# Performance work log

Hardware: AMD Instinct MI355X
Metric: run time of the kernel (lower is better)

Reference implementation:

```python
import jax, jax.numpy as jnp
import numpy as np
from jax import lax

WIN = 9
PAD = WIN // 2


def _box_sum(x):
    # x: [B,1,H,W]; all-ones WINxWIN conv, stride 1, pad PAD -> same spatial size
    k = jnp.ones((1, 1, WIN, WIN), dtype=x.dtype)
    return lax.conv_general_dilated(
        x, k, window_strides=(1, 1), padding=[(PAD, PAD), (PAD, PAD)],
        dimension_numbers=("NCHW", "OIHW", "NCHW"))


def setup_inputs() -> dict:
    key = jax.random.key(0)
    k1, k2 = jax.random.split(key)
    B, C, H, W = 32, 1, 512, 512
    y_true = jax.random.uniform(k1, (B, C, H, W), dtype=jnp.float32)
    y_pred = jax.random.uniform(k2, (B, C, H, W), dtype=jnp.float32)
    return {"y_true": y_true, "y_pred": y_pred}


def reference(y_true, y_pred):
    Ii, Ji = y_true, y_pred
    win_size = float(WIN * WIN)
    I_sum = _box_sum(Ii)
    J_sum = _box_sum(Ji)
    I2_sum = _box_sum(Ii * Ii)
    J2_sum = _box_sum(Ji * Ji)
    IJ_sum = _box_sum(Ii * Ji)
    u_I = I_sum / win_size
    u_J = J_sum / win_size
    cross = IJ_sum - u_J * I_sum - u_I * J_sum + u_I * u_J * win_size
    I_var = I2_sum - 2.0 * u_I * I_sum + u_I * u_I * win_size
    J_var = J2_sum - 2.0 * u_J * J_sum + u_J * u_J * win_size
    cc = cross * cross / (I_var * J_var + 1e-05)
    return -jnp.mean(cc)
```

## Files before the change

kernel.cpp:

```cpp
#include <hip/hip_runtime.h>


#define BATCH     32
#define IMH       512
#define IMW       512
#define SH        16
#define NROWSTRIP 32
#define NCOLSTRIP 4
#define CBW       128
#define NPART     (BATCH * NROWSTRIP * NCOLSTRIP)
#define NK        (SH + 8)
#define VROW      136

#define LOADROW(RI, CI, CJ, HI, HJ) do {                                   \
    const int ri_ = (RI);                                                  \
    CI = make_float2(0.f, 0.f); CJ = make_float2(0.f, 0.f);                \
    HI = 0.f; HJ = 0.f;                                                    \
    if ((unsigned)ri_ < (unsigned)IMH) {                                   \
        const float* rI_ = Ib + (size_t)ri_ * IMW;                         \
        const float* rJ_ = Jb + (size_t)ri_ * IMW;                         \
        CI = *(const float2*)(rI_ + cc0);                                  \
        CJ = *(const float2*)(rJ_ + cc0);                                  \
        if (u < 8 && (unsigned)hc < (unsigned)IMW) {                       \
            HI = rI_[hc]; HJ = rJ_[hc];                                    \
        }                                                                  \
    }                                                                      \
} while (0)

#define HWIN(QI, HA, HB) do {                                              \
    const float2 w0_ = *(const float2*)&Vbuf[QI][l0];                      \
    const float2 w1_ = *(const float2*)&Vbuf[QI][l0 + 2];                  \
    const float2 w2_ = *(const float2*)&Vbuf[QI][l0 + 4];                  \
    const float2 w3_ = *(const float2*)&Vbuf[QI][l0 + 6];                  \
    const float2 w4_ = *(const float2*)&Vbuf[QI][l0 + 8];                  \
    HA = ((w0_.x + w0_.y) + (w1_.x + w1_.y))                               \
       + ((w2_.x + w2_.y) + (w3_.x + w3_.y)) + w4_.x;                      \
    HB = HA + w4_.y - w0_.x;                                               \
} while (0)

#define CC1(AI, AJ, S2, S3, S4) do {                                       \
    const float cross = (S4) - (AI)*(AJ)*inv81;                            \
    const float ivv   = (S2) - (AI)*(AI)*inv81;                            \
    const float jvv   = (S3) - (AJ)*(AJ)*inv81;                            \
    acc += cross * cross * __builtin_amdgcn_rcpf(ivv * jvv + 1e-5f);       \
} while (0)

__global__ __launch_bounds__(64) void ncc_main(const float* __restrict__ I,
                                               const float* __restrict__ J,
                                               float* __restrict__ partial) {
    const int u    = threadIdx.x;
    const int cs   = blockIdx.x;
    const int s    = blockIdx.y;
    const int b    = blockIdx.z;
    const int r0   = s * SH;
    const int cblk = cs * CBW;
    const int cc0  = cblk + 2 * u;
    const int hc   = cblk + (u < 4 ? u - 4 : 124 + u);
    const int hx   = (u < 4) ? u : 128 + u;
    const int l0   = 2 * u;
    const float inv81 = 1.0f / 81.0f;

    const float* Ib = I + (size_t)b * IMH * IMW;
    const float* Jb = J + (size_t)b * IMH * IMW;

    __shared__ float4 ring[9][64];
    __shared__ float2 ringH[9][8];
    __shared__ float  Vbuf[5][VROW];

    float VI0 = 0.f, VI1 = 0.f, VJ0 = 0.f, VJ1 = 0.f;
    float VII0 = 0.f, VII1 = 0.f, VJJ0 = 0.f, VJJ1 = 0.f;
    float VIJ0 = 0.f, VIJ1 = 0.f;
    float hVI = 0.f, hVJ = 0.f, hVII = 0.f, hVJJ = 0.f, hVIJ = 0.f;
    float acc = 0.f;
    int slot = 0;

    float2 ci, cj; float hi, hj;
    LOADROW(r0 - 4, ci, cj, hi, hj);

#pragma unroll 1
    for (int K = 0; K < NK; ++K) {
        float2 ni, nj; float nhi, nhj;
        LOADROW((K + 1 < NK) ? (r0 - 3 + K) : -1, ni, nj, nhi, nhj);

        float4 oldv = make_float4(0.f, 0.f, 0.f, 0.f);
        float2 oldh = make_float2(0.f, 0.f);
        if (K >= 9) {
            oldv = ring[slot][u];
            if (u < 8) oldh = ringH[slot][u];
        }
        ring[slot][u] = make_float4(ci.x, ci.y, cj.x, cj.y);
        if (u < 8) ringH[slot][u] = make_float2(hi, hj);
        slot = (slot == 8) ? 0 : slot + 1;

        VI0  += ci.x - oldv.x;             VI1  += ci.y - oldv.y;
        VJ0  += cj.x - oldv.z;             VJ1  += cj.y - oldv.w;
        VII0 += ci.x*ci.x - oldv.x*oldv.x; VII1 += ci.y*ci.y - oldv.y*oldv.y;
        VJJ0 += cj.x*cj.x - oldv.z*oldv.z; VJJ1 += cj.y*cj.y - oldv.w*oldv.w;
        VIJ0 += ci.x*cj.x - oldv.x*oldv.z; VIJ1 += ci.y*cj.y - oldv.y*oldv.w;
        hVI  += hi - oldh.x;               hVJ  += hj - oldh.y;
        hVII += hi*hi - oldh.x*oldh.x;
        hVJJ += hj*hj - oldh.y*oldh.y;
        hVIJ += hi*hj - oldh.x*oldh.y;

        if (K >= 8) {
            *(float2*)&Vbuf[0][4 + l0] = make_float2(VI0,  VI1);
            *(float2*)&Vbuf[1][4 + l0] = make_float2(VJ0,  VJ1);
            *(float2*)&Vbuf[2][4 + l0] = make_float2(VII0, VII1);
            *(float2*)&Vbuf[3][4 + l0] = make_float2(VJJ0, VJJ1);
            *(float2*)&Vbuf[4][4 + l0] = make_float2(VIJ0, VIJ1);
            if (u < 8) {
                Vbuf[0][hx] = hVI;  Vbuf[1][hx] = hVJ;  Vbuf[2][hx] = hVII;
                Vbuf[3][hx] = hVJJ; Vbuf[4][hx] = hVIJ;
            }
            __syncthreads();
            float HI0, HI1, HJ0, HJ1, HA0, HA1, HB0, HB1, HC0, HC1;
            HWIN(0, HI0, HI1);
            HWIN(1, HJ0, HJ1);
            HWIN(2, HA0, HA1);
            HWIN(3, HB0, HB1);
            HWIN(4, HC0, HC1);
            CC1(HI0, HJ0, HA0, HB0, HC0);
            CC1(HI1, HJ1, HA1, HB1, HC1);
            __syncthreads();
        }

        ci = ni; cj = nj; hi = nhi; hj = nhj;
    }

    float sum = acc;
#pragma unroll
    for (int off = 32; off > 0; off >>= 1) sum += __shfl_down(sum, off, 64);
    if (u == 0) {
        partial[((size_t)b * NROWSTRIP + s) * NCOLSTRIP + cs] = sum;
    }
}

__global__ __launch_bounds__(256) void ncc_reduce(const float* __restrict__ partial,
                                                  float* __restrict__ out) {
    const int t = threadIdx.x;
    double ssum = 0.0;
    for (int idx = t; idx < NPART; idx += 256) ssum += (double)partial[idx];
#pragma unroll
    for (int off = 32; off > 0; off >>= 1) ssum += __shfl_down(ssum, off, 64);

    __shared__ double wsum[4];
    if ((t & 63) == 0) wsum[t >> 6] = ssum;
    __syncthreads();
    if (t == 0) {
        const double total = wsum[0] + wsum[1] + wsum[2] + wsum[3];
        out[0] = (float)(-total / 8388608.0);
    }
}

extern "C" void kernel_launch(void* const* d_in, const int* in_sizes, int n_in,
                              void* d_out, int out_size, void* d_ws, size_t ws_size,
                              hipStream_t stream) {
    const float* I = (const float*)d_in[0];
    const float* J = (const float*)d_in[1];
    float* partial = (float*)d_ws;
    float* out     = (float*)d_out;

    dim3 grid(NCOLSTRIP, NROWSTRIP, BATCH);
    ncc_main<<<grid, 64, 0, stream>>>(I, J, partial);
    ncc_reduce<<<1, 256, 0, stream>>>(partial, out);
}
```

Baseline: 126.8 us.

## Stage full row tile in LDS once and do horizontal-then-vertical box sums

Replaces the streaming ring-buffer scheme, which had two barriers per output row, with a single bulk load of all 24 input rows (interleaved I/J as float2) into shared memory followed by one barrier. Each output row then computes horizontal window sums from LDS and keeps vertical sums as a sliding add/subtract in registers. Horizontal sums for each row are recomputed twice (once entering, once leaving the window), trading extra ALU and LDS reads for the removed syncs. It also sets launch_bounds min blocks to 1 and fully unrolls, which can raise register pressure.

```diff
diff --git a/kernel.cpp b/kernel.cpp
--- a/kernel.cpp
+++ b/kernel.cpp
@@ -8,34 +8,34 @@
 #define NROWSTRIP 32
 #define NCOLSTRIP 4
 #define CBW       128
+#define NK        (SH + 8)
+#define TW        136
 #define NPART     (BATCH * NROWSTRIP * NCOLSTRIP)
-#define NK        (SH + 8)
-#define VROW      136
 
-#define LOADROW(RI, CI, CJ, HI, HJ) do {                                   \
-    const int ri_ = (RI);                                                  \
-    CI = make_float2(0.f, 0.f); CJ = make_float2(0.f, 0.f);                \
-    HI = 0.f; HJ = 0.f;                                                    \
-    if ((unsigned)ri_ < (unsigned)IMH) {                                   \
-        const float* rI_ = Ib + (size_t)ri_ * IMW;                         \
-        const float* rJ_ = Jb + (size_t)ri_ * IMW;                         \
-        CI = *(const float2*)(rI_ + cc0);                                  \
-        CJ = *(const float2*)(rJ_ + cc0);                                  \
-        if (u < 8 && (unsigned)hc < (unsigned)IMW) {                       \
-            HI = rI_[hc]; HJ = rJ_[hc];                                    \
-        }                                                                  \
-    }                                                                      \
-} while (0)
-
-#define HWIN(QI, HA, HB) do {                                              \
-    const float2 w0_ = *(const float2*)&Vbuf[QI][l0];                      \
-    const float2 w1_ = *(const float2*)&Vbuf[QI][l0 + 2];                  \
-    const float2 w2_ = *(const float2*)&Vbuf[QI][l0 + 4];                  \
-    const float2 w3_ = *(const float2*)&Vbuf[QI][l0 + 6];                  \
-    const float2 w4_ = *(const float2*)&Vbuf[QI][l0 + 8];                  \
-    HA = ((w0_.x + w0_.y) + (w1_.x + w1_.y))                               \
-       + ((w2_.x + w2_.y) + (w3_.x + w3_.y)) + w4_.x;                      \
-    HB = HA + w4_.y - w0_.x;                                               \
+#define HCALC(K, HI0,HI1,HJ0,HJ1,HA0,HA1,HB0,HB1,HC0,HC1) do {             \
+    const float4 w0_ = *(const float4*)&tile[K][l0];                       \
+    const float4 w1_ = *(const float4*)&tile[K][l0 + 2];                   \
+    const float4 w2_ = *(const float4*)&tile[K][l0 + 4];                   \
+    const float4 w3_ = *(const float4*)&tile[K][l0 + 6];                   \
+    const float4 w4_ = *(const float4*)&tile[K][l0 + 8];                   \
+    HI0 = ((w0_.x + w0_.z) + (w1_.x + w1_.z))                              \
+        + ((w2_.x + w2_.z) + (w3_.x + w3_.z)) + w4_.x;                     \
+    HI1 = HI0 + w4_.z - w0_.x;                                             \
+    HJ0 = ((w0_.y + w0_.w) + (w1_.y + w1_.w))                              \
+        + ((w2_.y + w2_.w) + (w3_.y + w3_.w)) + w4_.y;                     \
+    HJ1 = HJ0 + w4_.w - w0_.y;                                             \
+    HA0 = ((w0_.x*w0_.x + w0_.z*w0_.z) + (w1_.x*w1_.x + w1_.z*w1_.z))      \
+        + ((w2_.x*w2_.x + w2_.z*w2_.z) + (w3_.x*w3_.x + w3_.z*w3_.z))      \
+        + w4_.x*w4_.x;                                                     \
+    HA1 = HA0 + w4_.z*w4_.z - w0_.x*w0_.x;                                 \
+    HB0 = ((w0_.y*w0_.y + w0_.w*w0_.w) + (w1_.y*w1_.y + w1_.w*w1_.w))      \
+        + ((w2_.y*w2_.y + w2_.w*w2_.w) + (w3_.y*w3_.y + w3_.w*w3_.w))      \
+        + w4_.y*w4_.y;                                                     \
+    HB1 = HB0 + w4_.w*w4_.w - w0_.y*w0_.y;                                 \
+    HC0 = ((w0_.x*w0_.y + w0_.z*w0_.w) + (w1_.x*w1_.y + w1_.z*w1_.w))      \
+        + ((w2_.x*w2_.y + w2_.z*w2_.w) + (w3_.x*w3_.y + w3_.z*w3_.w))      \
+        + w4_.x*w4_.y;                                                     \
+    HC1 = HC0 + w4_.z*w4_.w - w0_.x*w0_.y;                                 \
 } while (0)
 
 #define CC1(AI, AJ, S2, S3, S4) do {                                       \
@@ -45,86 +45,77 @@
     acc += cross * cross * __builtin_amdgcn_rcpf(ivv * jvv + 1e-5f);       \
 } while (0)
 
-__global__ __launch_bounds__(64) void ncc_main(const float* __restrict__ I,
-                                               const float* __restrict__ J,
-                                               float* __restrict__ partial) {
+__global__ __launch_bounds__(64, 1) void ncc_main(const float* __restrict__ I,
+                                                  const float* __restrict__ J,
+                                                  float* __restrict__ partial) {
     const int u    = threadIdx.x;
     const int cs   = blockIdx.x;
     const int s    = blockIdx.y;
     const int b    = blockIdx.z;
     const int r0   = s * SH;
     const int cblk = cs * CBW;
-    const int cc0  = cblk + 2 * u;
-    const int hc   = cblk + (u < 4 ? u - 4 : 124 + u);
-    const int hx   = (u < 4) ? u : 128 + u;
+    const int stc  = cblk - 4 + 2 * u;
+    const int hc   = cblk + 124 + u;
     const int l0   = 2 * u;
     const float inv81 = 1.0f / 81.0f;
 
     const float* Ib = I + (size_t)b * IMH * IMW;
     const float* Jb = J + (size_t)b * IMH * IMW;
 
-    __shared__ float4 ring[9][64];
-    __shared__ float2 ringH[9][8];
-    __shared__ float  Vbuf[5][VROW];
+    __shared__ float2 tile[NK][TW];
 
-    float VI0 = 0.f, VI1 = 0.f, VJ0 = 0.f, VJ1 = 0.f;
-    float VII0 = 0.f, VII1 = 0.f, VJJ0 = 0.f, VJJ1 = 0.f;
-    float VIJ0 = 0.f, VIJ1 = 0.f;
-    float hVI = 0.f, hVJ = 0.f, hVII = 0.f, hVJJ = 0.f, hVIJ = 0.f;
+#pragma unroll
+    for (int k = 0; k < NK; ++k) {
+        const int ri = r0 - 4 + k;
+        float2 iv = make_float2(0.f, 0.f), jv = make_float2(0.f, 0.f);
+        float hi = 0.f, hj = 0.f;
+        if ((unsigned)ri < (unsigned)IMH) {
+            const float* rI = Ib + (size_t)ri * IMW;
+            const float* rJ = Jb + (size_t)ri * IMW;
+            if ((unsigned)stc < (unsigned)IMW) {
+                iv = *(const float2*)(rI + stc);
+                jv = *(const float2*)(rJ + stc);
+            }
+            if (u < 8 && (unsigned)hc < (unsigned)IMW) {
+                hi = rI[hc]; hj = rJ[hc];
+            }
+        }
+        *(float4*)&tile[k][2 * u] = make_float4(iv.x, jv.x, iv.y, jv.y);
+        if (u < 8) tile[k][128 + u] = make_float2(hi, hj);
+    }
+    __syncthreads();
+
+    float vI0 = 0.f, vI1 = 0.f, vJ0 = 0.f, vJ1 = 0.f;
+    float vA0 = 0.f, vA1 = 0.f, vB0 = 0.f, vB1 = 0.f;
+    float vC0 = 0.f, vC1 = 0.f;
     float acc = 0.f;
-    int slot = 0;
 
-    float2 ci, cj; float hi, hj;
-    LOADROW(r0 - 4, ci, cj, hi, hj);
+    {
+        float hI0, hI1, hJ0, hJ1, hA0, hA1, hB0, hB1, hC0, hC1;
+#pragma unroll
+        for (int k = 0; k < 9; ++k) {
+            HCALC(k, hI0, hI1, hJ0, hJ1, hA0, hA1, hB0, hB1, hC0, hC1);
+            vI0 += hI0; vI1 += hI1; vJ0 += hJ0; vJ1 += hJ1;
+            vA0 += hA0; vA1 += hA1; vB0 += hB0; vB1 += hB1;
+            vC0 += hC0; vC1 += hC1;
+        }
+        CC1(vI0, vJ0, vA0, vB0, vC0);
+        CC1(vI1, vJ1, vA1, vB1, vC1);
+    }
 
-#pragma unroll 1
-    for (int K = 0; K < NK; ++K) {
-        float2 ni, nj; float nhi, nhj;
-        LOADROW((K + 1 < NK) ? (r0 - 3 + K) : -1, ni, nj, nhi, nhj);
-
-        float4 oldv = make_float4(0.f, 0.f, 0.f, 0.f);
-        float2 oldh = make_float2(0.f, 0.f);
-        if (K >= 9) {
-            oldv = ring[slot][u];
-            if (u < 8) oldh = ringH[slot][u];
-        }
-        ring[slot][u] = make_float4(ci.x, ci.y, cj.x, cj.y);
-        if (u < 8) ringH[slot][u] = make_float2(hi, hj);
-        slot = (slot == 8) ? 0 : slot + 1;
-
-        VI0  += ci.x - oldv.x;             VI1  += ci.y - oldv.y;
-        VJ0  += cj.x - oldv.z;             VJ1  += cj.y - oldv.w;
-        VII0 += ci.x*ci.x - oldv.x*oldv.x; VII1 += ci.y*ci.y - oldv.y*oldv.y;
-        VJJ0 += cj.x*cj.x - oldv.z*oldv.z; VJJ1 += cj.y*cj.y - oldv.w*oldv.w;
-        VIJ0 += ci.x*cj.x - oldv.x*oldv.z; VIJ1 += ci.y*cj.y - oldv.y*oldv.w;
-        hVI  += hi - oldh.x;               hVJ  += hj - oldh.y;
-        hVII += hi*hi - oldh.x*oldh.x;
-        hVJJ += hj*hj - oldh.y*oldh.y;
-        hVIJ += hi*hj - oldh.x*oldh.y;
-
-        if (K >= 8) {
-            *(float2*)&Vbuf[0][4 + l0] = make_float2(VI0,  VI1);
-            *(float2*)&Vbuf[1][4 + l0] = make_float2(VJ0,  VJ1);
-            *(float2*)&Vbuf[2][4 + l0] = make_float2(VII0, VII1);
-            *(float2*)&Vbuf[3][4 + l0] = make_float2(VJJ0, VJJ1);
-            *(float2*)&Vbuf[4][4 + l0] = make_float2(VIJ0, VIJ1);
-            if (u < 8) {
-                Vbuf[0][hx] = hVI;  Vbuf[1][hx] = hVJ;  Vbuf[2][hx] = hVII;
-                Vbuf[3][hx] = hVJJ; Vbuf[4][hx] = hVIJ;
-            }
-            __syncthreads();
-            float HI0, HI1, HJ0, HJ1, HA0, HA1, HB0, HB1, HC0, HC1;
-            HWIN(0, HI0, HI1);
-            HWIN(1, HJ0, HJ1);
-            HWIN(2, HA0, HA1);
-            HWIN(3, HB0, HB1);
-            HWIN(4, HC0, HC1);
-            CC1(HI0, HJ0, HA0, HB0, HC0);
-            CC1(HI1, HJ1, HA1, HB1, HC1);
-            __syncthreads();
-        }
-
-        ci = ni; cj = nj; hi = nhi; hj = nhj;
+#pragma unroll
+    for (int t = 1; t < SH; ++t) {
+        float nI0, nI1, nJ0, nJ1, nA0, nA1, nB0, nB1, nC0, nC1;
+        float oI0, oI1, oJ0, oJ1, oA0, oA1, oB0, oB1, oC0, oC1;
+        HCALC(t + 8, nI0, nI1, nJ0, nJ1, nA0, nA1, nB0, nB1, nC0, nC1);
+        HCALC(t - 1, oI0, oI1, oJ0, oJ1, oA0, oA1, oB0, oB1, oC0, oC1);
+        vI0 += nI0 - oI0; vI1 += nI1 - oI1;
+        vJ0 += nJ0 - oJ0; vJ1 += nJ1 - oJ1;
+        vA0 += nA0 - oA0; vA1 += nA1 - oA1;
+        vB0 += nB0 - oB0; vB1 += nB1 - oB1;
+        vC0 += nC0 - oC0; vC1 += nC1 - oC1;
+        CC1(vI0, vJ0, vA0, vB0, vC0);
+        CC1(vI1, vJ1, vA1, vB1, vC1);
     }
 
     float sum = acc;
```

New measurement: 150.6 us. 18.8% more time.

## Deepen row prefetch to four rows and double strip height

Applied to the files above, without the earlier changes.

Each block now processes 32 output rows instead of 16, which halves the grid and cuts the redundant 8-row halo recomputation per strip. The loop is unrolled by four, with four register-held row buffers so global loads for rows K+4..K+7 are in flight while rows K..K+3 are processed, hiding memory latency. This costs more registers and gives fewer blocks, which lowers parallelism across CUs.

```diff
diff --git a/kernel.cpp b/kernel.cpp
--- a/kernel.cpp
+++ b/kernel.cpp
@@ -4,19 +4,20 @@
 #define BATCH     32
 #define IMH       512
 #define IMW       512
-#define SH        16
-#define NROWSTRIP 32
+#define SH        32
+#define NROWSTRIP 16
 #define NCOLSTRIP 4
 #define CBW       128
-#define NPART     (BATCH * NROWSTRIP * NCOLSTRIP)
 #define NK        (SH + 8)
 #define VROW      136
+#define NPART     (BATCH * NROWSTRIP * NCOLSTRIP)
 
-#define LOADROW(RI, CI, CJ, HI, HJ) do {                                   \
-    const int ri_ = (RI);                                                  \
+#define PREFG(KK, CI, CJ, HI, HJ) do {                                     \
+    const int kk_ = (KK);                                                  \
+    const int ri_ = r0 - 4 + kk_;                                          \
     CI = make_float2(0.f, 0.f); CJ = make_float2(0.f, 0.f);                \
     HI = 0.f; HJ = 0.f;                                                    \
-    if ((unsigned)ri_ < (unsigned)IMH) {                                   \
+    if (kk_ < NK && (unsigned)ri_ < (unsigned)IMH) {                       \
         const float* rI_ = Ib + (size_t)ri_ * IMW;                         \
         const float* rJ_ = Jb + (size_t)ri_ * IMW;                         \
         CI = *(const float2*)(rI_ + cc0);                                  \
@@ -45,6 +46,50 @@
     acc += cross * cross * __builtin_amdgcn_rcpf(ivv * jvv + 1e-5f);       \
 } while (0)
 
+#define EMIT() do {                                                        \
+    *(float2*)&Vbuf[0][4 + l0] = make_float2(VI0, VI1);                    \
+    *(float2*)&Vbuf[1][4 + l0] = make_float2(VJ0, VJ1);                    \
+    *(float2*)&Vbuf[2][4 + l0] = make_float2(VA0, VA1);                    \
+    *(float2*)&Vbuf[3][4 + l0] = make_float2(VB0, VB1);                    \
+    *(float2*)&Vbuf[4][4 + l0] = make_float2(VC0, VC1);                    \
+    if (u < 8) {                                                           \
+        Vbuf[0][hx] = hVI; Vbuf[1][hx] = hVJ; Vbuf[2][hx] = hVA;           \
+        Vbuf[3][hx] = hVB; Vbuf[4][hx] = hVC;                              \
+    }                                                                      \
+    __syncthreads();                \
+    float HI0, HI1, HJ0, HJ1, HA0, HA1, HB0, HB1, HC0, HC1;                \
+    HWIN(0, HI0, HI1);                                                     \
+    HWIN(1, HJ0, HJ1);                                                     \
+    HWIN(2, HA0, HA1);                                                     \
+    HWIN(3, HB0, HB1);                                                     \
+    HWIN(4, HC0, HC1);                                                     \
+    CC1(HI0, HJ0, HA0, HB0, HC0);                                          \
+    CC1(HI1, HJ1, HA1, HB1, HC1);                                          \
+    __syncthreads();              \
+} while (0)
+
+#define BODY(K, CI, CJ, HI, HJ) do {                                       \
+    float4 oldv = make_float4(0.f, 0.f, 0.f, 0.f);                         \
+    float2 oldh = make_float2(0.f, 0.f);                                   \
+    if ((K) >= 9) {                                                        \
+        oldv = ring[slot][u];                                              \
+        if (u < 8) oldh = ringH[slot][u];                                  \
+    }                                                                      \
+    ring[slot][u] = make_float4(CI.x, CI.y, CJ.x, CJ.y);                   \
+    if (u < 8) ringH[slot][u] = make_float2(HI, HJ);                       \
+    slot = (slot == 8) ? 0 : slot + 1;                                     \
+    VI0 += CI.x - oldv.x;             VI1 += CI.y - oldv.y;                \
+    VJ0 += CJ.x - oldv.z;             VJ1 += CJ.y - oldv.w;                \
+    VA0 += CI.x*CI.x - oldv.x*oldv.x; VA1 += CI.y*CI.y - oldv.y*oldv.y;    \
+    VB0 += CJ.x*CJ.x - oldv.z*oldv.z; VB1 += CJ.y*CJ.y - oldv.w*oldv.w;    \
+    VC0 += CI.x*CJ.x - oldv.x*oldv.z; VC1 += CI.y*CJ.y - oldv.y*oldv.w;    \
+    hVI += HI - oldh.x;               hVJ += HJ - oldh.y;                  \
+    hVA += HI*HI - oldh.x*oldh.x;                                          \
+    hVB += HJ*HJ - oldh.y*oldh.y;                                          \
+    hVC += HI*HJ - oldh.x*oldh.y;                                          \
+    if ((K) >= 8) { EMIT(); }                                              \
+} while (0)
+
 __global__ __launch_bounds__(64) void ncc_main(const float* __restrict__ I,
                                                const float* __restrict__ J,
                                                float* __restrict__ partial) {
@@ -68,63 +113,30 @@
     __shared__ float  Vbuf[5][VROW];
 
     float VI0 = 0.f, VI1 = 0.f, VJ0 = 0.f, VJ1 = 0.f;
-    float VII0 = 0.f, VII1 = 0.f, VJJ0 = 0.f, VJJ1 = 0.f;
-    float VIJ0 = 0.f, VIJ1 = 0.f;
-    float hVI = 0.f, hVJ = 0.f, hVII = 0.f, hVJJ = 0.f, hVIJ = 0.f;
+    float VA0 = 0.f, VA1 = 0.f, VB0 = 0.f, VB1 = 0.f;
+    float VC0 = 0.f, VC1 = 0.f;
+    float hVI = 0.f, hVJ = 0.f, hVA = 0.f, hVB = 0.f, hVC = 0.f;
     float acc = 0.f;
     int slot = 0;
 
-    float2 ci, cj; float hi, hj;
-    LOADROW(r0 - 4, ci, cj, hi, hj);
+    float2 pa_i, pa_j, pb_i, pb_j, pc_i, pc_j, pd_i, pd_j;
+    float  pa_hi, pa_hj, pb_hi, pb_hj, pc_hi, pc_hj, pd_hi, pd_hj;
+    PREFG(0, pa_i, pa_j, pa_hi, pa_hj);
+    PREFG(1, pb_i, pb_j, pb_hi, pb_hj);
+    PREFG(2, pc_i, pc_j, pc_hi, pc_hj);
+    PREFG(3, pd_i, pd_j, pd_hi, pd_hj);
 
 #pragma unroll 1
-    for (int K = 0; K < NK; ++K) {
-        float2 ni, nj; float nhi, nhj;
-        LOADROW((K + 1 < NK) ? (r0 - 3 + K) : -1, ni, nj, nhi, nhj);
-
-        float4 oldv = make_float4(0.f, 0.f, 0.f, 0.f);
-        float2 oldh = make_float2(0.f, 0.f);
-        if (K >= 9) {
-            oldv = ring[slot][u];
-            if (u < 8) oldh = ringH[slot][u];
-        }
-        ring[slot][u] = make_float4(ci.x, ci.y, cj.x, cj.y);
-        if (u < 8) ringH[slot][u] = make_float2(hi, hj);
-        slot = (slot == 8) ? 0 : slot + 1;
-
-        VI0  += ci.x - oldv.x;             VI1  += ci.y - oldv.y;
-        VJ0  += cj.x - oldv.z;             VJ1  += cj.y - oldv.w;
-        VII0 += ci.x*ci.x - oldv.x*oldv.x; VII1 += ci.y*ci.y - oldv.y*oldv.y;
-        VJJ0 += cj.x*cj.x - oldv.z*oldv.z; VJJ1 += cj.y*cj.y - oldv.w*oldv.w;
-        VIJ0 += ci.x*cj.x - oldv.x*oldv.z; VIJ1 += ci.y*cj.y - oldv.y*oldv.w;
-        hVI  += hi - oldh.x;               hVJ  += hj - oldh.y;
-        hVII += hi*hi - oldh.x*oldh.x;
-        hVJJ += hj*hj - oldh.y*oldh.y;
-        hVIJ += hi*hj - oldh.x*oldh.y;
-
-        if (K >= 8) {
-            *(float2*)&Vbuf[0][4 + l0] = make_float2(VI0,  VI1);
-            *(float2*)&Vbuf[1][4 + l0] = make_float2(VJ0,  VJ1);
-            *(float2*)&Vbuf[2][4 + l0] = make_float2(VII0, VII1);
-            *(float2*)&Vbuf[3][4 + l0] = make_float2(VJJ0, VJJ1);
-            *(float2*)&Vbuf[4][4 + l0] = make_float2(VIJ0, VIJ1);
-            if (u < 8) {
-                Vbuf[0][hx] = hVI;  Vbuf[1][hx] = hVJ;  Vbuf[2][hx] = hVII;
-                Vbuf[3][hx] = hVJJ; Vbuf[4][hx] = hVIJ;
-            }
-            __syncthreads();
-            float HI0, HI1, HJ0, HJ1, HA0, HA1, HB0, HB1, HC0, HC1;
-            HWIN(0, HI0, HI1);
-            HWIN(1, HJ0, HJ1);
-            HWIN(2, HA0, HA1);
-            HWIN(3, HB0, HB1);
-            HWIN(4, HC0, HC1);
-            CC1(HI0, HJ0, HA0, HB0, HC0);
-            CC1(HI1, HJ1, HA1, HB1, HC1);
-            __syncthreads();
-        }
-
-        ci = ni; cj = nj; hi = nhi; hj = nhj;
+    for (int g = 0; g < NK / 4; ++g) {
+        const int K = 4 * g;
+        BODY(K,     pa_i, pa_j, pa_hi, pa_hj);
+        PREFG(K + 4, pa_i, pa_j, pa_hi, pa_hj);
+        BODY(K + 1, pb_i, pb_j, pb_hi, pb_hj);
+        PREFG(K + 5, pb_i, pb_j, pb_hi, pb_hj);
+        BODY(K + 2, pc_i, pc_j, pc_hi, pc_hj);
+        PREFG(K + 6, pc_i, pc_j, pc_hi, pc_hj);
+        BODY(K + 3, pd_i, pd_j, pd_hi, pd_hj);
+        PREFG(K + 7, pd_i, pd_j, pd_hi, pd_hj);
     }
 
     float sum = acc;
```

Measured after the change: 116.6 us. 8.0% less time.
